# Optimization experiments

Measured on AMD Instinct MI355X. Metric: run time of the kernel, lower is better.

## Reference

```python
import jax, jax.numpy as jnp
import numpy as np

N, E, F_IN, D, L = 100000, 1600000, 32, 128, 5
B, V, T, EMB = 3000, 64, 128, 64
H = L * D  # 640 LSTM hidden
BN_EPS = 1e-5


def setup_inputs():
    key = jax.random.key(0)
    ks = jax.random.split(key, 20)
    rn = lambda k, s, sc=0.05: jax.random.normal(k, s, jnp.float32) * sc
    inp = {
        'x': jax.random.normal(ks[0], (N, F_IN), jnp.float32),
        'edge_index': jax.random.randint(ks[1], (2, E), 0, N, jnp.int32),
        'batch': jnp.sort(jax.random.randint(ks[2], (N,), 0, B, jnp.int32)),
        'smi': jax.random.randint(ks[3], (B, T), 0, V, jnp.int32),
        'gin0_w1': rn(ks[4], (F_IN, D)), 'gin0_b1': jnp.zeros((D,), jnp.float32),
        'gin0_w2': rn(ks[5], (D, D)),    'gin0_b2': jnp.zeros((D,), jnp.float32),
        'ginr_w1': rn(ks[6], (L - 1, D, D)), 'ginr_b1': jnp.zeros((L - 1, D), jnp.float32),
        'ginr_w2': rn(ks[7], (L - 1, D, D)), 'ginr_b2': jnp.zeros((L - 1, D), jnp.float32),
        'bn_gamma': jnp.ones((L, D), jnp.float32), 'bn_beta': jnp.zeros((L, D), jnp.float32),
        'emb': rn(ks[8], (V, EMB), 0.1).at[0].set(0.0),  # padding_idx=0
        'w_ih': rn(ks[9], (4 * H, EMB), 0.04), 'w_hh': rn(ks[10], (4 * H, H), 0.04),
        'b_ih': jnp.zeros((4 * H,), jnp.float32), 'b_hh': jnp.zeros((4 * H,), jnp.float32),
        'g_w1': rn(ks[11], (L * D, 4 * D)), 'g_b1': jnp.zeros((4 * D,), jnp.float32),
        'g_bn_gamma': jnp.ones((4 * D,), jnp.float32), 'g_bn_beta': jnp.zeros((4 * D,), jnp.float32),
        'g_w2': rn(ks[12], (4 * D, 6 * D)),
    }
    return inp


def _bn(h, gamma, beta):
    # BatchNorm1d in training mode: biased batch statistics
    mu = h.mean(0)
    var = h.var(0)
    return (h - mu) * jax.lax.rsqrt(var + BN_EPS) * gamma + beta


def _gin_layer(h, src, dst, w1, b1, w2, b2, gamma, beta):
    # GINConv (eps=0): MLP(x + sum_{j->i} x_j), then ReLU, then BN
    agg = jax.ops.segment_sum(h[src], dst, num_segments=N)  # [N, d]
    z = h + agg
    z = jnp.maximum(z @ w1 + b1, 0.0) @ w2 + b2
    z = jnp.maximum(z, 0.0)
    return _bn(z, gamma, beta)


def _lstm_last(e, w_ih, w_hh, b_ih, b_hh):
    # e: [B, T, EMB] -> last hidden state [B, H]
    def step(carry, xt):
        h, c = carry
        gates = xt @ w_ih.T + b_ih + h @ w_hh.T + b_hh  # [B, 4H]
        i, f, g, o = jnp.split(gates, 4, axis=1)  # torch gate order i,f,g,o
        c = jax.nn.sigmoid(f) * c + jax.nn.sigmoid(i) * jnp.tanh(g)
        h = jax.nn.sigmoid(o) * jnp.tanh(c)
        return (h, c), None
    h0 = jnp.zeros((e.shape[0], H), e.dtype)
    (h, _), _ = jax.lax.scan(step, (h0, h0), e.transpose(1, 0, 2))
    return h


def reference(x, edge_index, batch, smi, gin0_w1, gin0_b1, gin0_w2, gin0_b2,
              ginr_w1, ginr_b1, ginr_w2, ginr_b2, bn_gamma, bn_beta, emb,
              w_ih, w_hh, b_ih, b_hh, g_w1, g_b1, g_bn_gamma, g_bn_beta, g_w2):
    src, dst = edge_index[0], edge_index[1]
    # --- GIN encoder with layer-wise global_add_pool ---
    h = _gin_layer(x, src, dst, gin0_w1, gin0_b1, gin0_w2, gin0_b2, bn_gamma[0], bn_beta[0])
    pools = [jax.ops.segment_sum(h, batch, num_segments=B)]
    for i in range(L - 1):
        h = _gin_layer(h, src, dst, ginr_w1[i], ginr_b1[i], ginr_w2[i], ginr_b2[i],
                       bn_gamma[i + 1], bn_beta[i + 1])
        pools.append(jax.ops.segment_sum(h, batch, num_segments=B))
    enc1 = jnp.concatenate(pools, axis=1)  # [B, L*D]
    # --- SMILES encoder: Embedding + LSTM, take output at last timestep ---
    enc2 = _lstm_last(emb[smi], w_ih, w_hh, b_ih, b_hh)  # [B, H] == [B, L*D]
    # --- shared projection head g, L2-normalized (F.normalize, eps=1e-12) ---
    def g_head(z):
        z1 = jnp.maximum(_bn(z @ g_w1 + g_b1, g_bn_gamma, g_bn_beta), 0.0)
        out = z1 @ g_w2
        nrm = jnp.maximum(jnp.linalg.norm(out, axis=1, keepdims=True), 1e-12)
        return out / nrm
    return (g_head(enc1), g_head(enc2))
```

## Files before the change

### kernel.cpp

```cpp
#include <hip/hip_runtime.h>

typedef __bf16 bf16x8 __attribute__((ext_vector_type(8)));
typedef float f32x4 __attribute__((ext_vector_type(4)));
typedef unsigned short ushort8 __attribute__((ext_vector_type(8)));

#define DEV static __device__ __forceinline__

DEV unsigned short f2bf(float f){
  unsigned int u = __builtin_bit_cast(unsigned int, f);
  u += 0x7fffu + ((u >> 16) & 1u);
  return (unsigned short)(u >> 16);
}
DEV float bf2f(unsigned short u){
  return __builtin_bit_cast(float, ((unsigned int)u) << 16);
}
DEV float sigf(float x){ return 1.0f/(1.0f + __expf(-x)); }
DEV float tanhf_fast(float x){
  float ax = fabsf(x);
  float e = __expf(2.0f*ax);
  float r = 1.0f - 2.0f/(e + 1.0f);
  return copysignf(r, x);
}

static constexpr int NN   = 100000;
static constexpr int NPAD = 100096;
static constexpr int NE   = 1600000;
static constexpr int NB   = 3000;
static constexpr int BPAD = 3072;
static constexpr int TT   = 128;
static constexpr int HID  = 640;
static constexpr int SCAN_B = 1024;
static constexpr int NBLK = (NN + SCAN_B - 1)/SCAN_B;

__global__ void cvt_k(const float* __restrict__ s, unsigned short* __restrict__ d, int n){
  int i = blockIdx.x*256 + threadIdx.x; if (i < n) d[i] = f2bf(s[i]);
}
__global__ void transpose_cvt_split_k(const float* __restrict__ s, unsigned short* __restrict__ dh,
                                      unsigned short* __restrict__ dl, int R, int C){
  int i = blockIdx.x*256 + threadIdx.x; if (i >= R*C) return;
  int r = i / C, c = i - r*C;
  float v = s[i];
  unsigned short hi = f2bf(v);
  dh[c*R + r] = hi;
  dl[c*R + r] = f2bf(v - bf2f(hi));
}
__global__ void wc2_build_k(const float* __restrict__ whh, const float* __restrict__ wih,
                            unsigned short* __restrict__ wc2){
  int i = blockIdx.x*256 + threadIdx.x; if (i >= 2560*704) return;
  int n2 = i / 704, k = i - n2*704;
  int jt = n2 >> 7, rem = n2 & 127;
  int hc = rem >> 6, gate = (rem >> 4) & 3, j15 = rem & 15;
  int n = gate*640 + jt*32 + hc*16 + j15;
  float v = (k < 640) ? whh[n*640 + k] : wih[n*64 + (k - 640)];
  wc2[i] = f2bf(v);
}
__global__ void add_k(const float* __restrict__ a, const float* __restrict__ b, float* __restrict__ o, int n){
  int i = blockIdx.x*256 + threadIdx.x; if (i < n) o[i] = a[i] + b[i];
}

__global__ __launch_bounds__(256) void deg_hist_k(const int* __restrict__ dsts, int* __restrict__ deg){
  int e = blockIdx.x*256 + threadIdx.x; if (e < NE) atomicAdd(&deg[dsts[e]], 1);
}
__global__ __launch_bounds__(256) void scan_bsum_k(const int* __restrict__ deg, int* __restrict__ bsum){
  __shared__ int red[4];
  int b = blockIdx.x, tid = threadIdx.x;
  int base = b*SCAN_B + tid*4;
  int s = 0;
  #pragma unroll
  for (int q = 0; q < 4; ++q){ int idx = base + q; s += (idx < NN) ? deg[idx] : 0; }
  #pragma unroll
  for (int m = 1; m < 64; m <<= 1) s += __shfl_xor(s, m);
  if ((tid & 63) == 0) red[tid >> 6] = s;
  __syncthreads();
  if (tid == 0) bsum[b] = red[0] + red[1] + red[2] + red[3];
}
__global__ void scan_off_k(int* __restrict__ bsum){
  if (threadIdx.x == 0){
    int run = 0;
    for (int i = 0; i < NBLK; ++i){ int t = bsum[i]; bsum[i] = run; run += t; }
  }
}
__global__ __launch_bounds__(256) void scan_write_k(const int* __restrict__ deg, const int* __restrict__ bsum,
                                                    int* __restrict__ rowptr, int* __restrict__ cursor){
  __shared__ int tsum[256];
  int b = blockIdx.x, tid = threadIdx.x;
  int base = b*SCAN_B + tid*4;
  int v[4]; int s = 0;
  #pragma unroll
  for (int q = 0; q < 4; ++q){ int idx = base + q; v[q] = (idx < NN) ? deg[idx] : 0; s += v[q]; }
  tsum[tid] = s;
  __syncthreads();
  for (int offt = 1; offt < 256; offt <<= 1){
    int y = (tid >= offt) ? tsum[tid - offt] : 0;
    __syncthreads();
    tsum[tid] += y;
    __syncthreads();
  }
  int run = bsum[b] + tsum[tid] - s;
  #pragma unroll
  for (int q = 0; q < 4; ++q){
    int idx = base + q;
    if (idx < NN){ rowptr[idx] = run; cursor[idx] = run; }
    run += v[q];
  }
  if (b == 0 && tid == 0) rowptr[NN] = NE;
}
__global__ __launch_bounds__(256) void csr_fill_k(const int* __restrict__ srcs, const int* __restrict__ dsts,
                                                  int* __restrict__ cursor, int* __restrict__ eidx){
  int e = blockIdx.x*256 + threadIdx.x; if (e >= NE) return;
  int d = dsts[e];
  int pos = atomicAdd(&cursor[d], 1);
  eidx[pos] = srcs[e];
}

__global__ __launch_bounds__(256) void gbound_k(const int* __restrict__ batch, int* __restrict__ gstart){
  int i = blockIdx.x*256 + threadIdx.x;
  if (i >= NN) return;
  int bi = batch[i];
  int bp = (i == 0) ? -1 : batch[i-1];
  for (int g = bp + 1; g <= bi; ++g) gstart[g] = i;
  if (i == NN-1){
    for (int g = bi + 1; g <= NB; ++g) gstart[g] = NN;
  }
}

__global__ __launch_bounds__(256) void agg128_k(const int* __restrict__ rowptr, const int* __restrict__ eidx,
    const float* __restrict__ H, float* __restrict__ Z){
  int wid = (blockIdx.x*256 + threadIdx.x) >> 6;
  if (wid >= NN) return;
  int lane = threadIdx.x & 63;
  const float2* Hp = (const float2*)H;
  int n0 = rowptr[wid], n1 = rowptr[wid+1];
  float2 acc = Hp[(size_t)wid*64 + lane];
  int i = n0;
  for (; i + 1 < n1; i += 2){
    int s0 = eidx[i], s1 = eidx[i+1];
    float2 v0 = Hp[(size_t)s0*64 + lane];
    float2 v1 = Hp[(size_t)s1*64 + lane];
    acc.x += v0.x + v1.x; acc.y += v0.y + v1.y;
  }
  if (i < n1){
    float2 v = Hp[(size_t)eidx[i]*64 + lane];
    acc.x += v.x; acc.y += v.y;
  }
  ((float2*)Z)[(size_t)wid*64 + lane] = acc;
}
__global__ __launch_bounds__(256) void agg32_k(const int* __restrict__ rowptr, const int* __restrict__ eidx,
    const float* __restrict__ X, float* __restrict__ Z){
  int r = (blockIdx.x*256 + threadIdx.x) >> 5;
  if (r >= NN) return;
  int l = threadIdx.x & 31;
  int n0 = rowptr[r], n1 = rowptr[r+1];
  float acc = X[(size_t)r*32 + l];
  int i = n0;
  for (; i + 1 < n1; i += 2){
    int s0 = eidx[i], s1 = eidx[i+1];
    acc += X[(size_t)s0*32 + l] + X[(size_t)s1*32 + l];
  }
  if (i < n1) acc += X[(size_t)eidx[i]*32 + l];
  Z[(size_t)r*32 + l] = acc;
}

template<int KIN>
__global__ __launch_bounds__(256) void gin_mlp_k(const float* __restrict__ Z,
    const unsigned short* __restrict__ W1h, const unsigned short* __restrict__ W1l,
    const unsigned short* __restrict__ W2h, const unsigned short* __restrict__ W2l,
    const float* __restrict__ b1, const float* __restrict__ b2,
    float* __restrict__ Y, float* __restrict__ stats)
{
  constexpr int SA = KIN + 8;
  __shared__ __align__(16) unsigned short Ah[128*136];
  __shared__ __align__(16) unsigned short Al[128*136];
  const int tid = threadIdx.x, lane = tid & 63, w = tid >> 6;
  const int row0 = blockIdx.x * 128;
  const int wr = (w >> 1)*64, wc0 = (w & 1)*64;
  const int l15 = lane & 15, lg = lane >> 4;

  constexpr int CH = KIN/8;
  #pragma unroll
  for (int i = 0; i < (128*CH)/256; ++i){
    int chunk = tid + 256*i;
    int row = chunk / CH, kc = (chunk - row*CH)*8;
    const float* sp = Z + (size_t)(row0 + row)*KIN + kc;
    float4 a0 = *(const float4*)sp;
    float4 a1 = *(const float4*)(sp + 4);
    float vv[8] = {a0.x,a0.y,a0.z,a0.w,a1.x,a1.y,a1.z,a1.w};
    ushort8 vh, vl;
    #pragma unroll
    for (int q=0;q<8;++q){ unsigned short h = f2bf(vv[q]); vh[q]=h; vl[q]=f2bf(vv[q]-bf2f(h)); }
    *(ushort8*)&Ah[row*SA + kc] = vh;
    *(ushort8*)&Al[row*SA + kc] = vl;
  }
  __syncthreads();

  f32x4 acc[4][4];
  #pragma unroll
  for (int i=0;i<4;++i)
    #pragma unroll
    for (int j=0;j<4;++j) acc[i][j] = (f32x4)(0.0f);

  #pragma unroll
  for (int k0 = 0; k0 < KIN; k0 += 32){
    bf16x8 ah[4], al[4], bh[4], bl[4];
    #pragma unroll
    for (int fa=0; fa<4; ++fa){
      ah[fa] = *(const bf16x8*)&Ah[(wr + fa*16 + l15)*SA + k0 + 8*lg];
      al[fa] = *(const bf16x8*)&Al[(wr + fa*16 + l15)*SA + k0 + 8*lg];
    }
    #pragma unroll
    for (int fb=0; fb<4; ++fb){
      bh[fb] = *(const bf16x8*)&W1h[(wc0 + fb*16 + l15)*KIN + k0 + 8*lg];
      bl[fb] = *(const bf16x8*)&W1l[(wc0 + fb*16 + l15)*KIN + k0 + 8*lg];
    }
    #pragma unroll
    for (int fa=0; fa<4; ++fa)
      #pragma unroll
      for (int fb=0; fb<4; ++fb){
        acc[fa][fb] = __builtin_amdgcn_mfma_f32_16x16x32_bf16(ah[fa], bh[fb], acc[fa][fb], 0, 0, 0);
        acc[fa][fb] = __builtin_amdgcn_mfma_f32_16x16x32_bf16(al[fa], bh[fb], acc[fa][fb], 0, 0, 0);
        acc[fa][fb] = __builtin_amdgcn_mfma_f32_16x16x32_bf16(ah[fa], bl[fb], acc[fa][fb], 0, 0, 0);
      }
  }
  __syncthreads();

  {
    float b1v[4];
    #pragma unroll
    for (int fb=0; fb<4; ++fb) b1v[fb] = b1[wc0 + fb*16 + l15];
    #pragma unroll
    for (int fa=0; fa<4; ++fa)
      #pragma unroll
      for (int fb=0; fb<4; ++fb)
        #pragma unroll
        for (int r=0; r<4; ++r){
          float v = fmaxf(acc[fa][fb][r] + b1v[fb], 0.0f);
          unsigned short h = f2bf(v);
          int idx = (wr + fa*16 + lg*4 + r)*136 + (wc0 + fb*16 + l15);
          Ah[idx] = h;
          Al[idx] = f2bf(v - bf2f(h));
        }
  }
  __syncthreads();

  f32x4 acc2[4][4];
  #pragma unroll
  for (int i=0;i<4;++i)
    #pragma unroll
    for (int j=0;j<4;++j) acc2[i][j] = (f32x4)(0.0f);

  #pragma unroll
  for (int k0 = 0; k0 < 128; k0 += 32){
    bf16x8 ah[4], al[4], bh[4], bl[4];
    #pragma unroll
    for (int fa=0; fa<4; ++fa){
      ah[fa] = *(const bf16x8*)&Ah[(wr + fa*16 + l15)*136 + k0 + 8*lg];
      al[fa] = *(const bf16x8*)&Al[(wr + fa*16 + l15)*136 + k0 + 8*lg];
    }
    #pragma unroll
    for (int fb=0; fb<4; ++fb){
      bh[fb] = *(const bf16x8*)&W2h[(wc0 + fb*16 + l15)*128 + k0 + 8*lg];
      bl[fb] = *(const bf16x8*)&W2l[(wc0 + fb*16 + l15)*128 + k0 + 8*lg];
    }
    #pragma unroll
    for (int fa=0; fa<4; ++fa)
      #pragma unroll
      for (int fb=0; fb<4; ++fb){
        acc2[fa][fb] = __builtin_amdgcn_mfma_f32_16x16x32_bf16(ah[fa], bh[fb], acc2[fa][fb], 0, 0, 0);
        acc2[fa][fb] = __builtin_amdgcn_mfma_f32_16x16x32_bf16(al[fa], bh[fb], acc2[fa][fb], 0, 0, 0);
        acc2[fa][fb] = __builtin_amdgcn_mfma_f32_16x16x32_bf16(ah[fa], bl[fb], acc2[fa][fb], 0, 0, 0);
      }
  }

  float b2v[4]; int cc[4];
  #pragma unroll
  for (int fb=0; fb<4; ++fb){ cc[fb] = wc0 + fb*16 + l15; b2v[fb] = b2[cc[fb]]; }
  float ps[4] = {0,0,0,0}, pq[4] = {0,0,0,0};
  #pragma unroll
  for (int fa=0; fa<4; ++fa)
    #pragma unroll
    for (int fb=0; fb<4; ++fb)
      #pragma unroll
      for (int r=0; r<4; ++r){
        int row = row0 + wr + fa*16 + lg*4 + r;
        float v = fmaxf(acc2[fa][fb][r] + b2v[fb], 0.0f);
        if (row < NN){
          Y[(size_t)row*128 + cc[fb]] = v;
          ps[fb] += v; pq[fb] += v*v;
        }
      }
  #pragma unroll
  for (int fb=0; fb<4; ++fb){
    float s = ps[fb]; s += __shfl_xor(s, 16); s += __shfl_xor(s, 32);
    float q = pq[fb]; q += __shfl_xor(q, 16); q += __shfl_xor(q, 32);
    if (lane < 16){ atomicAdd(&stats[cc[fb]], s); atomicAdd(&stats[128 + cc[fb]], q); }
  }
}

__global__ void bn_finalize_k(const float* __restrict__ stats, const float* __restrict__ gamma,
                              const float* __restrict__ beta, float* __restrict__ sshift, int C, float invN){
  int c = blockIdx.x*blockDim.x + threadIdx.x; if (c >= C) return;
  float mean = stats[c]*invN;
  float var  = fmaxf(stats[C+c]*invN - mean*mean, 0.0f);
  float inv  = rsqrtf(var + 1e-5f);
  float sc   = gamma[c]*inv;
  sshift[c] = sc; sshift[C+c] = beta[c] - mean*sc;
}

__global__ __launch_bounds__(256) void bn_pool_k(const float* __restrict__ Y,
    const float* __restrict__ sshift, const int* __restrict__ gstart,
    float* __restrict__ Hb, float* __restrict__ pool, int layer)
{
  int g = blockIdx.x*4 + (threadIdx.x >> 6);
  if (g >= NB) return;
  int lane = threadIdx.x & 63;
  int c0 = lane << 1;
  float sc0 = sshift[c0],     sc1 = sshift[c0+1];
  float sh0 = sshift[128+c0], sh1 = sshift[128+c0+1];
  int n0 = gstart[g], n1 = gstart[g+1];
  const float2* Yp = (const float2*)Y;
  float2* Hp = (float2*)Hb;
  float2 acc = make_float2(0.f, 0.f);
  for (int r = n0; r < n1; ++r){
    float2 y = Yp[(size_t)r*64 + lane];
    float2 h = make_float2(y.x*sc0 + sh0, y.y*sc1 + sh1);
    Hp[(size_t)r*64 + lane] = h;
    acc.x += h.x; acc.y += h.y;
  }
  ((float2*)pool)[(size_t)g*320 + layer*64 + lane] = acc;
}

__global__ __launch_bounds__(256) void embed_k(const int* __restrict__ smi,
    const unsigned short* __restrict__ emb_bf, unsigned short* __restrict__ e2){
  int gid = blockIdx.x*256 + threadIdx.x;
  int tb = gid >> 4;
  if (tb >= TT*BPAD) return;
  int t = tb / BPAD, b = tb - t*BPAD;
  int k4 = (gid & 15) << 2;
  uint2 v = make_uint2(0u, 0u);
  if (b < NB){
    int tok = smi[b*TT + t];
    v = *(const uint2*)&emb_bf[tok*64 + k4];
  }
  *(uint2*)&e2[(size_t)tb*64 + k4] = v;
}

__global__ __launch_bounds__(256) void lstm_step_k(const unsigned short* __restrict__ hprev,
    unsigned short* __restrict__ hnext, float* __restrict__ cbuf,
    const unsigned short* __restrict__ e2, const unsigned short* __restrict__ Wc2,
    const float* __restrict__ biasc, int t, float* __restrict__ hfin)
{
  __shared__ __align__(16) unsigned short As[2][128*40];
  __shared__ __align__(16) unsigned short Bs[2][128*40];
  const int tid = threadIdx.x, lane = tid & 63, w = tid >> 6;
  const int row0 = blockIdx.x * 128;
  const int jt = blockIdx.y;
  const int l15 = lane & 15, lg = lane >> 4;
  const int wr = (w >> 1)*64, wc0 = (w & 1)*64;

  const int srow = tid >> 2, skc = (tid & 3) << 3;
  const unsigned short* A0 = hprev + (size_t)(row0 + srow)*HID;
  const unsigned short* A1 = hprev + (size_t)(row0 + srow + 64)*HID;
  const unsigned short* E0 = e2 + ((size_t)t*BPAD + row0 + srow)*64;
  const unsigned short* E1 = e2 + ((size_t)t*BPAD + row0 + srow + 64)*64;
  const unsigned short* B0 = Wc2 + (size_t)(jt*128 + srow)*704;
  const unsigned short* B1 = Wc2 + (size_t)(jt*128 + srow + 64)*704;

  *(ushort8*)&As[0][srow*40 + skc]      = *(const ushort8*)&A0[skc];
  *(ushort8*)&As[0][(srow+64)*40 + skc] = *(const ushort8*)&A1[skc];
  *(ushort8*)&Bs[0][srow*40 + skc]      = *(const ushort8*)&B0[skc];
  *(ushort8*)&Bs[0][(srow+64)*40 + skc] = *(const ushort8*)&B1[skc];
  __syncthreads();

  f32x4 acc[4][4];
  #pragma unroll
  for (int i=0;i<4;++i)
    #pragma unroll
    for (int j=0;j<4;++j) acc[i][j] = (f32x4)(0.0f);

  int p = 0;
  for (int kk = 0; kk < 22; ++kk){
    ushort8 va0, va1, vb0, vb1;
    const int k1 = (kk+1)*32;
    if (kk < 21){
      if (k1 < 640){
        va0 = *(const ushort8*)&A0[k1 + skc];
        va1 = *(const ushort8*)&A1[k1 + skc];
      } else {
        va0 = *(const ushort8*)&E0[k1 - 640 + skc];
        va1 = *(const ushort8*)&E1[k1 - 640 + skc];
      }
      vb0 = *(const ushort8*)&B0[k1 + skc];
      vb1 = *(const ushort8*)&B1[k1 + skc];
    }
    bf16x8 a[4], b[4];
    #pragma unroll
    for (int fa=0; fa<4; ++fa) a[fa] = *(const bf16x8*)&As[p][(wr + fa*16 + l15)*40 + 8*lg];
    #pragma unroll
    for (int fb=0; fb<4; ++fb) b[fb] = *(const bf16x8*)&Bs[p][(wc0 + fb*16 + l15)*40 + 8*lg];
    __builtin_amdgcn_s_setprio(1);
    #pragma unroll
    for (int fa=0; fa<4; ++fa)
      #pragma unroll
      for (int fb=0; fb<4; ++fb)
        acc[fa][fb] = __builtin_amdgcn_mfma_f32_16x16x32_bf16(a[fa], b[fb], acc[fa][fb], 0, 0, 0);
    __builtin_amdgcn_s_setprio(0);
    if (kk < 21){
      *(ushort8*)&As[p^1][srow*40 + skc]      = va0;
      *(ushort8*)&As[p^1][(srow+64)*40 + skc] = va1;
      *(ushort8*)&Bs[p^1][srow*40 + skc]      = vb0;
      *(ushort8*)&Bs[p^1][(srow+64)*40 + skc] = vb1;
    }
    __syncthreads();
    p ^= 1;
  }

  const int j = jt*32 + (w & 1)*16 + l15;
  float bi = biasc[j], bf_ = biasc[640+j], bg = biasc[1280+j], bo = biasc[1920+j];
  #pragma unroll
  for (int fa=0; fa<4; ++fa){
    #pragma unroll
    for (int r=0; r<4; ++r){
      int br = row0 + wr + fa*16 + lg*4 + r;
      float iv = acc[fa][0][r] + bi;
      float fv = acc[fa][1][r] + bf_;
      float gv = acc[fa][2][r] + bg;
      float ov = acc[fa][3][r] + bo;
      size_t idx = (size_t)br*HID + j;
      float co = cbuf[idx];
      float cn = sigf(fv)*co + sigf(iv)*tanhf_fast(gv);
      cbuf[idx] = cn;
      float hv = sigf(ov)*tanhf_fast(cn);
      hnext[idx] = f2bf(hv);
      if (hfin) hfin[idx] = hv;
    }
  }
}

template<int DO_STATS>
__global__ __launch_bounds__(256) void gemm_split_k(const float* __restrict__ A,
    const unsigned short* __restrict__ Bh, const unsigned short* __restrict__ Bl,
    const float* __restrict__ bias, float* __restrict__ outp, float* __restrict__ stats,
    int Mvalid, int Nc, int K)
{
  __shared__ __align__(16) unsigned short Ah[128*40];
  __shared__ __align__(16) unsigned short Al[128*40];
  const int tid = threadIdx.x, lane = tid & 63, w = tid >> 6;
  const int row0 = blockIdx.x * 128, col0 = blockIdx.y * 128;
  const int wr = (w >> 1)*64, wc0 = (w & 1)*64;
  const int l15 = lane & 15, lg = lane >> 4;

  f32x4 acc[4][4];
  #pragma unroll
  for (int i=0;i<4;++i)
    #pragma unroll
    for (int j=0;j<4;++j) acc[i][j] = (f32x4)(0.0f);

  for (int k0 = 0; k0 < K; k0 += 32){
    #pragma unroll
    for (int i=0;i<2;++i){
      int chunk = tid + 256*i;
      int row = chunk >> 2, kc = (chunk & 3) << 3;
      const float* sp = A + (size_t)(row0+row)*K + k0 + kc;
      float4 a0 = *(const float4*)sp;
      float4 a1 = *(const float4*)(sp + 4);
      float vv[8] = {a0.x,a0.y,a0.z,a0.w,a1.x,a1.y,a1.z,a1.w};
      ushort8 vh, vl;
      #pragma unroll
      for (int q=0;q<8;++q){ unsigned short h = f2bf(vv[q]); vh[q]=h; vl[q]=f2bf(vv[q]-bf2f(h)); }
      *(ushort8*)&Ah[row*40 + kc] = vh;
      *(ushort8*)&Al[row*40 + kc] = vl;
    }
    __syncthreads();
    bf16x8 ah[4], al[4], bh[4], bl[4];
    #pragma unroll
    for (int fa=0; fa<4; ++fa){
      ah[fa] = *(const bf16x8*)&Ah[(wr + fa*16 + l15)*40 + 8*lg];
      al[fa] = *(const bf16x8*)&Al[(wr + fa*16 + l15)*40 + 8*lg];
    }
    #pragma unroll
    for (int fb=0; fb<4; ++fb){
      bh[fb] = *(const bf16x8*)&Bh[(size_t)(col0 + wc0 + fb*16 + l15)*K + k0 + 8*lg];
      bl[fb] = *(const bf16x8*)&Bl[(size_t)(col0 + wc0 + fb*16 + l15)*K + k0 + 8*lg];
    }
    #pragma unroll
    for (int fa=0; fa<4; ++fa)
      #pragma unroll
      for (int fb=0; fb<4; ++fb){
        acc[fa][fb] = __builtin_amdgcn_mfma_f32_16x16x32_bf16(ah[fa], bh[fb], acc[fa][fb], 0, 0, 0);
        acc[fa][fb] = __builtin_amdgcn_mfma_f32_16x16x32_bf16(al[fa], bh[fb], acc[fa][fb], 0, 0, 0);
        acc[fa][fb] = __builtin_amdgcn_mfma_f32_16x16x32_bf16(ah[fa], bl[fb], acc[fa][fb], 0, 0, 0);
      }
    __syncthreads();
  }

  float bv[4]; int cc[4];
  #pragma unroll
  for (int fb=0; fb<4; ++fb){ cc[fb] = col0 + wc0 + fb*16 + l15; bv[fb] = bias ? bias[cc[fb]] : 0.0f; }
  float ps[4] = {0,0,0,0}, pq[4] = {0,0,0,0};
  #pragma unroll
  for (int fa=0; fa<4; ++fa)
    #pragma unroll
    for (int fb=0; fb<4; ++fb)
      #pragma unroll
      for (int r=0; r<4; ++r){
        int row = row0 + wr + fa*16 + lg*4 + r;
        float v = acc[fa][fb][r] + bv[fb];
        if (row < Mvalid){
          outp[(size_t)row*Nc + cc[fb]] = v;
          if (DO_STATS){ ps[fb] += v; pq[fb] += v*v; }
        }
      }
  if (DO_STATS){
    #pragma unroll
    for (int fb=0; fb<4; ++fb){
      float s = ps[fb]; s += __shfl_xor(s, 16); s += __shfl_xor(s, 32);
      float q = pq[fb]; q += __shfl_xor(q, 16); q += __shfl_xor(q, 32);
      if (lane < 16){ atomicAdd(&stats[cc[fb]], s); atomicAdd(&stats[Nc + cc[fb]], q); }
    }
  }
}

__global__ __launch_bounds__(256) void bn_apply_head_k(const float* __restrict__ Zpre,
    const float* __restrict__ sshift, float* __restrict__ z1f){
  int gid = blockIdx.x*256 + threadIdx.x;
  int r = gid >> 7;
  if (r >= BPAD) return;
  int c0 = (gid & 127) << 2;
  float4 o = make_float4(0.f,0.f,0.f,0.f);
  if (r < NB){
    float4 v = *(const float4*)&Zpre[(size_t)r*512 + c0];
    o.x = fmaxf(v.x*sshift[c0+0] + sshift[512+c0+0], 0.0f);
    o.y = fmaxf(v.y*sshift[c0+1] + sshift[512+c0+1], 0.0f);
    o.z = fmaxf(v.z*sshift[c0+2] + sshift[512+c0+2], 0.0f);
    o.w = fmaxf(v.w*sshift[c0+3] + sshift[512+c0+3], 0.0f);
  }
  *(float4*)&z1f[(size_t)r*512 + c0] = o;
}

__global__ __launch_bounds__(256) void rownorm_k(const float* __restrict__ in, float* __restrict__ outp){
  int r = blockIdx.x;
  const float* p = in + (size_t)r*768;
  float ss = 0.0f;
  #pragma unroll
  for (int i = 0; i < 3; ++i){ float v = p[threadIdx.x + 256*i]; ss += v*v; }
  #pragma unroll
  for (int m = 1; m < 64; m <<= 1) ss += __shfl_xor(ss, m);
  __shared__ float red[4];
  if ((threadIdx.x & 63) == 0) red[threadIdx.x >> 6] = ss;
  __syncthreads();
  float tot = red[0] + red[1] + red[2] + red[3];
  float inv = 1.0f / fmaxf(sqrtf(tot), 1e-12f);
  float* q = outp + (size_t)r*768;
  #pragma unroll
  for (int i = 0; i < 3; ++i) q[threadIdx.x + 256*i] = p[threadIdx.x + 256*i]*inv;
}

static inline int cdiv(long a, long b){ return (int)((a + b - 1)/b); }

extern "C" void kernel_launch(void* const* d_in, const int* in_sizes, int n_in,
                              void* d_out, int out_size, void* d_ws, size_t ws_size,
                              hipStream_t stream)
{
  const float* x        = (const float*)d_in[0];
  const int*   edges    = (const int*)d_in[1];
  const int*   batch    = (const int*)d_in[2];
  const int*   smi      = (const int*)d_in[3];
  const float* gin0_w1  = (const float*)d_in[4];
  const float* gin0_b1  = (const float*)d_in[5];
  const float* gin0_w2  = (const float*)d_in[6];
  const float* gin0_b2  = (const float*)d_in[7];
  const float* ginr_w1  = (const float*)d_in[8];
  const float* ginr_b1  = (const float*)d_in[9];
  const float* ginr_w2  = (const float*)d_in[10];
  const float* ginr_b2  = (const float*)d_in[11];
  const float* bn_gamma = (const float*)d_in[12];
  const float* bn_beta  = (const float*)d_in[13];
  const float* emb      = (const float*)d_in[14];
  const float* w_ih     = (const float*)d_in[15];
  const float* w_hh     = (const float*)d_in[16];
  const float* b_ih     = (const float*)d_in[17];
  const float* b_hh     = (const float*)d_in[18];
  const float* g_w1     = (const float*)d_in[19];
  const float* g_b1     = (const float*)d_in[20];
  const float* g_bng    = (const float*)d_in[21];
  const float* g_bnb    = (const float*)d_in[22];
  const float* g_w2     = (const float*)d_in[23];
  float* outp = (float*)d_out;
  const int* srcs = edges;
  const int* dsts = edges + NE;

  char* base = (char*)d_ws;
  size_t off = 0;
  auto carve = [&](size_t bytes)->char*{ char* p = base + off; off += (bytes + 255) & ~(size_t)255; return p; };
  float* z_gin = (float*)carve((size_t)NPAD*128*4);
  float* y_gin = (float*)carve((size_t)NPAD*128*4);
  float* h_gin = (float*)carve((size_t)NPAD*128*4);
  float* pool  = (float*)carve((size_t)BPAD*HID*4);
  unsigned short* Wc2    = (unsigned short*)carve((size_t)2560*704*2);
  float*          biasc  = (float*)carve(2560*4);
  unsigned short* emb_bf = (unsigned short*)carve(4096*2);
  unsigned short* w1t0h  = (unsigned short*)carve(128*32*2);
  unsigned short* w1t0l  = (unsigned short*)carve(128*32*2);
  unsigned short* w2t0h  = (unsigned short*)carve(128*128*2);
  unsigned short* w2t0l  = (unsigned short*)carve(128*128*2);
  unsigned short* w1trh  = (unsigned short*)carve(4*16384*2);
  unsigned short* w1trl  = (unsigned short*)carve(4*16384*2);
  unsigned short* w2trh  = (unsigned short*)carve(4*16384*2);
  unsigned short* w2trl  = (unsigned short*)carve(4*16384*2);
  unsigned short* gw1th  = (unsigned short*)carve(512*640*2);
  unsigned short* gw1tl  = (unsigned short*)carve(512*640*2);
  unsigned short* gw2th  = (unsigned short*)carve(768*512*2);
  unsigned short* gw2tl  = (unsigned short*)carve(768*512*2);
  float* stats  = (float*)carve(1024*4);
  float* sshift = (float*)carve(1024*4);
  int* deg    = (int*)carve((size_t)NN*4);
  int* cursor = (int*)carve((size_t)NN*4);
  int* rowptr = (int*)carve((size_t)(NN+1)*4);
  int* bsum   = (int*)carve(512);
  int* eidx   = (int*)carve((size_t)NE*4);
  int* gstart = (int*)carve((size_t)(NB+1)*4);

  unsigned short* e2     = (unsigned short*)y_gin;
  unsigned short* h_a    = (unsigned short*)h_gin;
  unsigned short* h_b    = h_a + (size_t)BPAD*HID;
  float*          c_buf  = (float*)(h_b + (size_t)BPAD*HID);
  float*          hfin   = c_buf + (size_t)BPAD*HID;
  float*          z1pre  = (float*)z_gin;
  float*          z1f    = z1pre + (size_t)BPAD*512;
  float*          outtmp = z1f + (size_t)BPAD*512;

  wc2_build_k<<<cdiv((long)2560*704,256),256,0,stream>>>(w_hh, w_ih, Wc2);
  add_k<<<cdiv(2560,256),256,0,stream>>>(b_ih, b_hh, biasc, 2560);
  cvt_k<<<cdiv(4096,256),256,0,stream>>>(emb, emb_bf, 4096);
  transpose_cvt_split_k<<<cdiv(32*128,256),256,0,stream>>>(gin0_w1, w1t0h, w1t0l, 32, 128);
  transpose_cvt_split_k<<<cdiv(16384,256),256,0,stream>>>(gin0_w2, w2t0h, w2t0l, 128, 128);
  for (int i = 0; i < 4; ++i){
    transpose_cvt_split_k<<<cdiv(16384,256),256,0,stream>>>(ginr_w1 + (size_t)i*16384, w1trh + (size_t)i*16384, w1trl + (size_t)i*16384, 128, 128);
    transpose_cvt_split_k<<<cdiv(16384,256),256,0,stream>>>(ginr_w2 + (size_t)i*16384, w2trh + (size_t)i*16384, w2trl + (size_t)i*16384, 128, 128);
  }
  transpose_cvt_split_k<<<cdiv(640*512,256),256,0,stream>>>(g_w1, gw1th, gw1tl, 640, 512);
  transpose_cvt_split_k<<<cdiv(512*768,256),256,0,stream>>>(g_w2, gw2th, gw2tl, 512, 768);

  hipMemsetAsync(deg, 0, (size_t)NN*4, stream);
  deg_hist_k<<<cdiv(NE,256),256,0,stream>>>(dsts, deg);
  scan_bsum_k<<<NBLK,256,0,stream>>>(deg, bsum);
  scan_off_k<<<1,64,0,stream>>>(bsum);
  scan_write_k<<<NBLK,256,0,stream>>>(deg, bsum, rowptr, cursor);
  csr_fill_k<<<cdiv(NE,256),256,0,stream>>>(srcs, dsts, cursor, eidx);
  gbound_k<<<cdiv(NN,256),256,0,stream>>>(batch, gstart);

  for (int l = 0; l < 5; ++l){
    hipMemsetAsync(stats, 0, 1024*4, stream);
    if (l == 0)
      agg32_k<<<cdiv((long)NN*32,256),256,0,stream>>>(rowptr, eidx, x, z_gin);
    else
      agg128_k<<<cdiv((long)NN*64,256),256,0,stream>>>(rowptr, eidx, h_gin, z_gin);
    if (l == 0)
      gin_mlp_k<32><<<NPAD/128,256,0,stream>>>(z_gin, w1t0h, w1t0l, w2t0h, w2t0l, gin0_b1, gin0_b2, y_gin, stats);
    else
      gin_mlp_k<128><<<NPAD/128,256,0,stream>>>(z_gin, w1trh + (size_t)(l-1)*16384, w1trl + (size_t)(l-1)*16384,
                                                w2trh + (size_t)(l-1)*16384, w2trl + (size_t)(l-1)*16384,
                                                ginr_b1 + (l-1)*128, ginr_b2 + (l-1)*128, y_gin, stats);
    bn_finalize_k<<<1,128,0,stream>>>(stats, bn_gamma + l*128, bn_beta + l*128, sshift, 128, 1.0f/NN);
    bn_pool_k<<<cdiv(NB,4),256,0,stream>>>(y_gin, sshift, gstart, h_gin, pool, l);
  }

  embed_k<<<cdiv((long)TT*BPAD*16,256),256,0,stream>>>(smi, emb_bf, e2);
  hipMemsetAsync(h_a, 0, (size_t)BPAD*HID*2, stream);
  hipMemsetAsync(c_buf, 0, (size_t)BPAD*HID*4, stream);
  for (int t = 0; t < TT; ++t){
    const unsigned short* hin = (t & 1) ? h_b : h_a;
    unsigned short* hout      = (t & 1) ? h_a : h_b;
    lstm_step_k<<<dim3(BPAD/128, 20),256,0,stream>>>(hin, hout, c_buf, e2, Wc2, biasc, t,
                                                     (t == TT-1) ? hfin : nullptr);
  }

  const float* headAf[2] = { pool, hfin };
  for (int hd = 0; hd < 2; ++hd){
    hipMemsetAsync(stats, 0, 1024*4, stream);
    gemm_split_k<1><<<dim3(BPAD/128, 4),256,0,stream>>>(headAf[hd], gw1th, gw1tl, g_b1, z1pre, stats, NB, 512, 640);
    bn_finalize_k<<<2,256,0,stream>>>(stats, g_bng, g_bnb, sshift, 512, 1.0f/NB);
    bn_apply_head_k<<<cdiv((long)BPAD*128,256),256,0,stream>>>(z1pre, sshift, z1f);
    gemm_split_k<0><<<dim3(BPAD/128, 6),256,0,stream>>>(z1f, gw2th, gw2tl, nullptr, outtmp, nullptr, NB, 768, 512);
    rownorm_k<<<NB,256,0,stream>>>(outtmp, outp + (size_t)hd*NB*768);
  }
}
```

Baseline: 4.373 ms.

## Give each wave private LDS tiles in LSTM step to drop block barriers

Each of the four waves now stages its own 64-row A and B slices into a private double-buffered LDS region, so the per-k-step __syncthreads in the LSTM recurrence GEMM can be removed. Tiles shared between waves are loaded redundantly, which doubles global and LDS traffic and doubles LDS usage per block. In exchange the waves no longer stall on each other at every k-step. Correctness relies on each wave staging exactly the rows it reads, with ordering inside a wave handled implicitly.

After: 5.187 ms. 1.19x slower.

```diff
diff --git a/kernel.cpp b/kernel.cpp
--- a/kernel.cpp
+++ b/kernel.cpp
@@ -349,27 +349,28 @@
     const unsigned short* __restrict__ e2, const unsigned short* __restrict__ Wc2,
     const float* __restrict__ biasc, int t, float* __restrict__ hfin)
 {
-  __shared__ __align__(16) unsigned short As[2][128*40];
-  __shared__ __align__(16) unsigned short Bs[2][128*40];
+  __shared__ __align__(16) unsigned short Aw[4][2][64*40];
+  __shared__ __align__(16) unsigned short Bw[4][2][64*40];
   const int tid = threadIdx.x, lane = tid & 63, w = tid >> 6;
   const int row0 = blockIdx.x * 128;
   const int jt = blockIdx.y;
   const int l15 = lane & 15, lg = lane >> 4;
   const int wr = (w >> 1)*64, wc0 = (w & 1)*64;
 
-  const int srow = tid >> 2, skc = (tid & 3) << 3;
-  const unsigned short* A0 = hprev + (size_t)(row0 + srow)*HID;
-  const unsigned short* A1 = hprev + (size_t)(row0 + srow + 64)*HID;
-  const unsigned short* E0 = e2 + ((size_t)t*BPAD + row0 + srow)*64;
-  const unsigned short* E1 = e2 + ((size_t)t*BPAD + row0 + srow + 64)*64;
-  const unsigned short* B0 = Wc2 + (size_t)(jt*128 + srow)*704;
-  const unsigned short* B1 = Wc2 + (size_t)(jt*128 + srow + 64)*704;
-
-  *(ushort8*)&As[0][srow*40 + skc]      = *(const ushort8*)&A0[skc];
-  *(ushort8*)&As[0][(srow+64)*40 + skc] = *(const ushort8*)&A1[skc];
-  *(ushort8*)&Bs[0][srow*40 + skc]      = *(const ushort8*)&B0[skc];
-  *(ushort8*)&Bs[0][(srow+64)*40 + skc] = *(const ushort8*)&B1[skc];
-  __syncthreads();
+  const int srow = lane >> 2, skc = (lane & 3) << 3;
+  const unsigned short* Abase = hprev + (size_t)(row0 + wr)*HID;
+  const unsigned short* Ebase = e2 + ((size_t)t*BPAD + row0 + wr)*64;
+  const unsigned short* Bbase = Wc2 + (size_t)(jt*128 + wc0)*704;
+
+  unsigned short* Amy = &Aw[w][0][0];
+  unsigned short* Bmy = &Bw[w][0][0];
+
+  #pragma unroll
+  for (int i = 0; i < 4; ++i){
+    int row = srow + 16*i;
+    *(ushort8*)&Amy[row*40 + skc] = *(const ushort8*)&Abase[(size_t)row*HID + skc];
+    *(ushort8*)&Bmy[row*40 + skc] = *(const ushort8*)&Bbase[(size_t)row*704 + skc];
+  }
 
   f32x4 acc[4][4];
   #pragma unroll
@@ -379,24 +380,24 @@
 
   int p = 0;
   for (int kk = 0; kk < 22; ++kk){
-    ushort8 va0, va1, vb0, vb1;
+    ushort8 va[4], vb[4];
     const int k1 = (kk+1)*32;
     if (kk < 21){
-      if (k1 < 640){
-        va0 = *(const ushort8*)&A0[k1 + skc];
-        va1 = *(const ushort8*)&A1[k1 + skc];
-      } else {
-        va0 = *(const ushort8*)&E0[k1 - 640 + skc];
-        va1 = *(const ushort8*)&E1[k1 - 640 + skc];
+      #pragma unroll
+      for (int i = 0; i < 4; ++i){
+        int row = srow + 16*i;
+        va[i] = (k1 < 640) ? *(const ushort8*)&Abase[(size_t)row*HID + k1 + skc]
+                           : *(const ushort8*)&Ebase[(size_t)row*64 + (k1 - 640) + skc];
+        vb[i] = *(const ushort8*)&Bbase[(size_t)row*704 + k1 + skc];
       }
-      vb0 = *(const ushort8*)&B0[k1 + skc];
-      vb1 = *(const ushort8*)&B1[k1 + skc];
-    }
+    }
+    const unsigned short* Ap = Amy + p*(64*40);
+    const unsigned short* Bp = Bmy + p*(64*40);
     bf16x8 a[4], b[4];
     #pragma unroll
-    for (int fa=0; fa<4; ++fa) a[fa] = *(const bf16x8*)&As[p][(wr + fa*16 + l15)*40 + 8*lg];
-    #pragma unroll
-    for (int fb=0; fb<4; ++fb) b[fb] = *(const bf16x8*)&Bs[p][(wc0 + fb*16 + l15)*40 + 8*lg];
+    for (int fa=0; fa<4; ++fa) a[fa] = *(const bf16x8*)&Ap[(fa*16 + l15)*40 + 8*lg];
+    #pragma unroll
+    for (int fb=0; fb<4; ++fb) b[fb] = *(const bf16x8*)&Bp[(fb*16 + l15)*40 + 8*lg];
     __builtin_amdgcn_s_setprio(1);
     #pragma unroll
     for (int fa=0; fa<4; ++fa)
@@ -405,12 +406,15 @@
         acc[fa][fb] = __builtin_amdgcn_mfma_f32_16x16x32_bf16(a[fa], b[fb], acc[fa][fb], 0, 0, 0);
     __builtin_amdgcn_s_setprio(0);
     if (kk < 21){
-      *(ushort8*)&As[p^1][srow*40 + skc]      = va0;
-      *(ushort8*)&As[p^1][(srow+64)*40 + skc] = va1;
-      *(ushort8*)&Bs[p^1][srow*40 + skc]      = vb0;
-      *(ushort8*)&Bs[p^1][(srow+64)*40 + skc] = vb1;
-    }
-    __syncthreads();
+      unsigned short* An = Amy + (p^1)*(64*40);
+      unsigned short* Bn = Bmy + (p^1)*(64*40);
+      #pragma unroll
+      for (int i = 0; i < 4; ++i){
+        int row = srow + 16*i;
+        *(ushort8*)&An[row*40 + skc] = va[i];
+        *(ushort8*)&Bn[row*40 + skc] = vb[i];
+      }
+    }
     p ^= 1;
   }
 
```
